# Kernel optimization log

Measured on AMD Instinct MI355X. Metric: run time of the kernel, lower is better.

## Reference

```python
import jax, jax.numpy as jnp
import numpy as np

DIM = 1024
HEADS = 16
HEAD_DIM = DIM // HEADS  # 64
EPS = 1e-5


def layer_norm(x, w, b):
    # LayerNorm over last dim (head_dim), matching nn.LayerNorm defaults
    mu = jnp.mean(x, axis=-1, keepdims=True)
    var = jnp.mean(jnp.square(x - mu), axis=-1, keepdims=True)
    return (x - mu) * jax.lax.rsqrt(var + EPS) * w + b


def apply_rotary_emb(x, freqs):
    # x: [B, S, H, D]; freqs: [S, D/2] angles. Interleaved (complex) rotary:
    # pairs (x[2i], x[2i+1]) rotated by angle freqs[:, i].
    x1 = x[..., 0::2]
    x2 = x[..., 1::2]
    cos = jnp.cos(freqs)[None, :, None, :]
    sin = jnp.sin(freqs)[None, :, None, :]
    r1 = x1 * cos - x2 * sin
    r2 = x1 * sin + x2 * cos
    return jnp.stack([r1, r2], axis=-1).reshape(x.shape)


def setup_inputs() -> dict:
    key = jax.random.key(0)
    ks = jax.random.split(key, 8)
    B, S = 2, 2048
    x = jax.random.normal(ks[0], (B, S, DIM), dtype=jnp.float32)
    freqs = jax.random.uniform(ks[1], (S, HEAD_DIM // 2), dtype=jnp.float32)
    sc = 1.0 / np.sqrt(DIM)
    w_qkv = jax.random.normal(ks[2], (DIM, 4 * DIM), dtype=jnp.float32) * sc
    w_out = jax.random.normal(ks[3], (DIM, DIM), dtype=jnp.float32) * sc
    qn_w = jnp.ones((HEAD_DIM,), jnp.float32)
    qn_b = jnp.zeros((HEAD_DIM,), jnp.float32)
    kn_w = jnp.ones((HEAD_DIM,), jnp.float32)
    kn_b = jnp.zeros((HEAD_DIM,), jnp.float32)
    return {"x": x, "freqs": freqs, "w_qkv": w_qkv, "w_out": w_out,
            "qn_w": qn_w, "qn_b": qn_b, "kn_w": kn_w, "kn_b": kn_b}


def reference(x, freqs, w_qkv, w_out, qn_w, qn_b, kn_w, kn_b):
    B, S, _ = x.shape
    qkv = x @ w_qkv  # [B, S, 4*DIM]
    q, k, v, gate = jnp.split(qkv, 4, axis=-1)
    q = q.reshape(B, S, HEADS, HEAD_DIM)
    k = k.reshape(B, S, HEADS, HEAD_DIM)
    v = v.reshape(B, S, HEADS, HEAD_DIM)
    q = layer_norm(q, qn_w, qn_b)
    k = layer_norm(k, kn_w, kn_b)
    q = apply_rotary_emb(q, freqs)
    k = apply_rotary_emb(k, freqs)
    # flash_attn_func: non-causal softmax attention, scale 1/sqrt(head_dim)
    scale = 1.0 / np.sqrt(HEAD_DIM)
    scores = jnp.einsum('bqhd,bkhd->bhqk', q, k) * scale
    probs = jax.nn.softmax(scores, axis=-1)
    o = jnp.einsum('bhqk,bkhd->bqhd', probs, v)
    o = o.reshape(B, S, DIM)
    o = o * jax.nn.sigmoid(gate)
    return o @ w_out
```

## Files before the change

kernel.cpp:

```cpp
#include <hip/hip_runtime.h>


typedef _Float16 f16;
typedef _Float16 f16x8 __attribute__((ext_vector_type(8)));
typedef _Float16 f16x4 __attribute__((ext_vector_type(4)));
typedef float    f32x4 __attribute__((ext_vector_type(4)));

#define MFMA16(a, b, c) __builtin_amdgcn_mfma_f32_16x16x32_f16((a), (b), (c), 0, 0, 0)

__device__ __forceinline__ void gload16(const void* g, void* l) {
  __builtin_amdgcn_global_load_lds(
      (const __attribute__((address_space(1))) void*)g,
      (__attribute__((address_space(3))) void*)l, 16, 0, 0);
}

__device__ __forceinline__ float exp2_fast(float x) {
#if __has_builtin(__builtin_amdgcn_exp2f)
  return __builtin_amdgcn_exp2f(x);
#else
  float r;
  asm("v_exp_f32 %0, %1" : "=v"(r) : "v"(x));
  return r;
#endif
}
__device__ __forceinline__ unsigned pkrtz(float a, float b) {
  typedef __fp16 hf16x2 __attribute__((ext_vector_type(2)));
  union { hf16x2 h; unsigned u; } c;
  c.h = __builtin_amdgcn_cvt_pkrtz(a, b);
  return c.u;
}

__global__ void rope_table_kernel(const float* __restrict__ freqs, float* __restrict__ tbl) {
  int i = blockIdx.x * 256 + threadIdx.x;
  if (i >= 2048 * 32) return;
  int s = i >> 5, j = i & 31;
  float f = freqs[i];
  tbl[s * 64 + j]      = cosf(f);
  tbl[s * 64 + 32 + j] = sinf(f);
}

__global__ void cast_f16_kernel(const float* __restrict__ in, f16* __restrict__ out, int n8) {
  int i = blockIdx.x * 256 + threadIdx.x;
  if (i >= n8) return;
  float4 a = ((const float4*)in)[2 * i];
  float4 b = ((const float4*)in)[2 * i + 1];
  f16x8 o;
  o[0] = (f16)a.x; o[1] = (f16)a.y; o[2] = (f16)a.z; o[3] = (f16)a.w;
  o[4] = (f16)b.x; o[5] = (f16)b.y; o[6] = (f16)b.z; o[7] = (f16)b.w;
  ((f16x8*)out)[i] = o;
}

__global__ void transpose_cast_kernel(const float* __restrict__ in, f16* __restrict__ out,
                                      int R, int C) {
  __shared__ float t[64][65];
  int c0 = blockIdx.x * 64, r0 = blockIdx.y * 64;
  int tx = threadIdx.x & 15, ty = threadIdx.x >> 4;
#pragma unroll
  for (int i = 0; i < 4; ++i) {
    float4 v = *(const float4*)&in[(size_t)(r0 + ty + 16 * i) * C + c0 + tx * 4];
    t[ty + 16 * i][tx * 4 + 0] = v.x;
    t[ty + 16 * i][tx * 4 + 1] = v.y;
    t[ty + 16 * i][tx * 4 + 2] = v.z;
    t[ty + 16 * i][tx * 4 + 3] = v.w;
  }
  __syncthreads();
#pragma unroll
  for (int i = 0; i < 4; ++i) {
    int n = c0 + ty + 16 * i;
    int k = r0 + tx * 4;
    f16x4 o;
    o[0] = (f16)t[tx * 4 + 0][ty + 16 * i];
    o[1] = (f16)t[tx * 4 + 1][ty + 16 * i];
    o[2] = (f16)t[tx * 4 + 2][ty + 16 * i];
    o[3] = (f16)t[tx * 4 + 3][ty + 16 * i];
    *(f16x4*)&out[(size_t)n * R + k] = o;
  }
}

__global__ void fill_debug_kernel(float* out, int n) {
  int i = blockIdx.x * 256 + threadIdx.x;
  if (i < n) out[i] = 12345.0f;
}

__global__ __launch_bounds__(512, 1) void gemm_qkv_256(
    const f16* __restrict__ A, const f16* __restrict__ B, int K,
    f16* __restrict__ qraw, f16* __restrict__ kraw,
    f16* __restrict__ g16, f16* __restrict__ v_t) {
  __shared__ f16 sA[2][256 * 64], sB[2][256 * 64];
  const int tid = threadIdx.x, lane = tid & 63;
  const int wave = tid >> 6;
  const int wm = wave >> 2, wn = wave & 3;
  const int lg = lane >> 4, lr = lane & 15;
  const int n0 = blockIdx.x * 256, m0 = blockIdx.y * 256;

  auto stg = [&](int k0, int p) {
#pragma unroll
    for (int r = 0; r < 4; ++r) {
      int off = (tid + r * 512) * 16;
      int row = off >> 7;
      int col = ((off & 127) ^ ((row & 7) << 4)) >> 1;
      gload16(A + (size_t)(m0 + row) * K + k0 + col, (char*)sA[p] + off);
      gload16(B + (size_t)(n0 + row) * K + k0 + col, (char*)sB[p] + off);
    }
  };

  f32x4 acc[8][4];
#pragma unroll
  for (int m = 0; m < 8; ++m)
#pragma unroll
    for (int n = 0; n < 4; ++n) acc[m][n] = (f32x4){0.f, 0.f, 0.f, 0.f};

  stg(0, 0);
  const int NT = K >> 6;
  int cur = 0;
  for (int t = 0; t < NT; ++t, cur ^= 1) {
    __syncthreads();
    if (t + 1 < NT) stg((t + 1) << 6, cur ^ 1);
#pragma unroll
    for (int ks = 0; ks < 2; ++ks) {
      f16x8 bfr[4];
#pragma unroll
      for (int n = 0; n < 4; ++n) {
        int row = wn * 64 + n * 16 + lr;
        int boff = (row << 7) + (ks << 6) + (lg << 4);
        boff ^= (row & 7) << 4;
        bfr[n] = *(const f16x8*)((const char*)sB[cur] + boff);
      }
#pragma unroll
      for (int m = 0; m < 8; ++m) {
        int row = wm * 128 + m * 16 + lr;
        int aoff = (row << 7) + (ks << 6) + (lg << 4);
        aoff ^= (row & 7) << 4;
        f16x8 afr = *(const f16x8*)((const char*)sA[cur] + aoff);
#pragma unroll
        for (int n = 0; n < 4; ++n) acc[m][n] = MFMA16(afr, bfr[n], acc[m][n]);
      }
    }
  }

  const int region = n0 >> 10;
  if (region == 2) {
#pragma unroll
    for (int m = 0; m < 8; ++m) {
      int row = m0 + wm * 128 + m * 16 + 4 * lg;
#pragma unroll
      for (int n = 0; n < 4; ++n) {
        int c = (n0 & 1023) + wn * 64 + n * 16 + lr;
        int hh = c >> 6, d = c & 63;
        int bb = row >> 11, s = row & 2047;
        f16x4 pv;
        pv[0] = (f16)acc[m][n][0];
        pv[1] = (f16)acc[m][n][1];
        pv[2] = (f16)acc[m][n][2];
        pv[3] = (f16)acc[m][n][3];
        *(f16x4*)&v_t[(size_t)((bb * 16 + hh) * 64 + d) * 2048 + s] = pv;
      }
    }
  } else if (region == 3) {
#pragma unroll
    for (int m = 0; m < 8; ++m) {
      int row = m0 + wm * 128 + m * 16 + 4 * lg;
#pragma unroll
      for (int n = 0; n < 4; ++n) {
        int col = (n0 & 1023) + wn * 64 + n * 16 + lr;
#pragma unroll
        for (int r = 0; r < 4; ++r) {
          float sg = 1.0f / (1.0f + exp2_fast(acc[m][n][r] * -1.44269504f));
          g16[(size_t)(row + r) * 1024 + col] = (f16)sg;
        }
      }
    }
  } else {
    f16* dst = region ? kraw : qraw;
#pragma unroll
    for (int m = 0; m < 8; ++m) {
      int row = m0 + wm * 128 + m * 16 + 4 * lg;
#pragma unroll
      for (int n = 0; n < 4; ++n) {
        int col = (n0 & 1023) + wn * 64 + n * 16 + lr;
#pragma unroll
        for (int r = 0; r < 4; ++r)
          dst[(size_t)(row + r) * 1024 + col] = (f16)acc[m][n][r];
      }
    }
  }
}

__global__ __launch_bounds__(256, 2) void gemm_out_128(
    const f16* __restrict__ A, const f16* __restrict__ B,
    float* __restrict__ Cout, int M, int N, int K) {
  __shared__ f16 sA[2][128 * 64], sB[2][128 * 64];
  const int tid = threadIdx.x, lane = tid & 63;
  const int wave = tid >> 6, wm = wave >> 1, wn = wave & 1;
  const int lg = lane >> 4, lr = lane & 15;
  const int n0 = blockIdx.x * 128, m0 = blockIdx.y * 128;

  auto stg = [&](int k0, int p) {
#pragma unroll
    for (int r = 0; r < 4; ++r) {
      int off = (tid + r * 256) * 16;
      int row = off >> 7;
      int col = ((off & 127) ^ ((row & 7) << 4)) >> 1;
      gload16(A + (size_t)(m0 + row) * K + k0 + col, (char*)sA[p] + off);
      gload16(B + (size_t)(n0 + row) * K + k0 + col, (char*)sB[p] + off);
    }
  };

  f32x4 acc[4][4];
#pragma unroll
  for (int m = 0; m < 4; ++m)
#pragma unroll
    for (int n = 0; n < 4; ++n) acc[m][n] = (f32x4){0.f, 0.f, 0.f, 0.f};

  stg(0, 0);
  const int NT = K >> 6;
  int cur = 0;
  for (int t = 0; t < NT; ++t, cur ^= 1) {
    __syncthreads();
    if (t + 1 < NT) stg((t + 1) << 6, cur ^ 1);
#pragma unroll
    for (int ks = 0; ks < 2; ++ks) {
      f16x8 bfr[4];
#pragma unroll
      for (int n = 0; n < 4; ++n) {
        int row = wn * 64 + n * 16 + lr;
        int boff = (row << 7) + (ks << 6) + (lg << 4);
        boff ^= (row & 7) << 4;
        bfr[n] = *(const f16x8*)((const char*)sB[cur] + boff);
      }
#pragma unroll
      for (int m = 0; m < 4; ++m) {
        int row = wm * 64 + m * 16 + lr;
        int aoff = (row << 7) + (ks << 6) + (lg << 4);
        aoff ^= (row & 7) << 4;
        f16x8 afr = *(const f16x8*)((const char*)sA[cur] + aoff);
#pragma unroll
        for (int n = 0; n < 4; ++n) acc[m][n] = MFMA16(afr, bfr[n], acc[m][n]);
      }
    }
  }

#pragma unroll
  for (int m = 0; m < 4; ++m) {
    int row = m0 + wm * 64 + m * 16 + 4 * lg;
#pragma unroll
    for (int n = 0; n < 4; ++n) {
      int col = n0 + wn * 64 + n * 16 + lr;
#pragma unroll
      for (int r = 0; r < 4; ++r) Cout[(size_t)(row + r) * N + col] = acc[m][n][r];
    }
  }
}

__global__ void norm_rope16_kernel(const f16* __restrict__ qr, const f16* __restrict__ kr,
                                   const float* __restrict__ tbl,
                                   const float* __restrict__ qn_w, const float* __restrict__ qn_b,
                                   const float* __restrict__ kn_w, const float* __restrict__ kn_b,
                                   f16* __restrict__ q_h, f16* __restrict__ k_h) {
  int row = blockIdx.x;
  int s = row & 2047;
  int hh = threadIdx.x >> 4, sub = threadIdx.x & 15;
  int base = row * 1024 + hh * 64 + sub * 4;
  float c0 = tbl[s * 64 + sub * 2 + 0], c1 = tbl[s * 64 + sub * 2 + 1];
  float s0 = tbl[s * 64 + 32 + sub * 2 + 0], s1 = tbl[s * 64 + 32 + sub * 2 + 1];
#pragma unroll
  for (int which = 0; which < 2; ++which) {
    const f16* src = which ? kr : qr;
    const float* wp = which ? kn_w : qn_w;
    const float* bp = which ? kn_b : qn_b;
    f16* dst = which ? k_h : q_h;
    f16x4 xr = *(const f16x4*)&src[base];
    float x0 = (float)xr[0], x1 = (float)xr[1], x2 = (float)xr[2], x3 = (float)xr[3];
    float sum = x0 + x1 + x2 + x3;
    sum += __shfl_xor(sum, 1); sum += __shfl_xor(sum, 2);
    sum += __shfl_xor(sum, 4); sum += __shfl_xor(sum, 8);
    float mu = sum * (1.0f / 64.0f);
    float d0 = x0 - mu, d1 = x1 - mu, d2 = x2 - mu, d3 = x3 - mu;
    float sq = d0 * d0 + d1 * d1 + d2 * d2 + d3 * d3;
    sq += __shfl_xor(sq, 1); sq += __shfl_xor(sq, 2);
    sq += __shfl_xor(sq, 4); sq += __shfl_xor(sq, 8);
    float rstd = rsqrtf(sq * (1.0f / 64.0f) + 1e-5f);
    float4 w = *(const float4*)&wp[sub * 4];
    float4 bb = *(const float4*)&bp[sub * 4];
    float n0 = d0 * rstd * w.x + bb.x;
    float n1 = d1 * rstd * w.y + bb.y;
    float n2 = d2 * rstd * w.z + bb.z;
    float n3 = d3 * rstd * w.w + bb.w;
    float r0 = n0 * c0 - n1 * s0, r1 = n0 * s0 + n1 * c0;
    float r2 = n2 * c1 - n3 * s1, r3 = n2 * s1 + n3 * c1;
    f16x4 ov;
    ov[0] = (f16)r0; ov[1] = (f16)r1; ov[2] = (f16)r2; ov[3] = (f16)r3;
    *(f16x4*)&dst[base] = ov;
  }
}

__global__ __launch_bounds__(256, 2) void attn_kernel(const f16* __restrict__ q_h,
                                                      const f16* __restrict__ k_h,
                                                      const f16* __restrict__ v_t,
                                                      const f16* __restrict__ g16,
                                                      f16* __restrict__ a16) {
  __shared__ __align__(16) char smem[65536];
  const int tid = threadIdx.x, lane = tid & 63, wave = tid >> 6;
  const int lg = lane >> 4, lr = lane & 15;
  const int bh = blockIdx.x >> 4, qt = blockIdx.x & 15;
  const int b = bh >> 4, h = bh & 15;
  const int qrow0 = b * 2048 + qt * 128 + wave * 32;

  auto stage = [&](int kv0, int p) {
    char* kb = smem + p * 16384;
    char* vb = smem + 32768 + p * 16384;
#pragma unroll
    for (int r = 0; r < 4; ++r) {
      int off = (tid + r * 256) * 16;
      {
        int row = off >> 7;
        int col = ((off & 127) ^ ((row & 7) << 4)) >> 1;
        int g = ((row >> 5) << 5) + (((row >> 2) & 3) << 3) + (((row >> 4) & 1) << 2) + (row & 3);
        gload16(&k_h[(size_t)(b * 2048 + kv0 + g) * 1024 + h * 64 + col], kb + off);
      }
      {
        int d = off >> 8;
        int col = ((off & 255) ^ ((d & 15) << 4)) >> 1;
        gload16(&v_t[(size_t)(bh * 64 + d) * 2048 + kv0 + col], vb + off);
      }
    }
  };

  f16x8 qf[2][2];
#pragma unroll
  for (int n = 0; n < 2; ++n)
#pragma unroll
    for (int ks = 0; ks < 2; ++ks)
      qf[n][ks] = *(const f16x8*)&q_h[(size_t)(qrow0 + n * 16 + lr) * 1024 + h * 64 + ks * 32 + lg * 8];

  f16x8 ones;
#pragma unroll
  for (int j = 0; j < 8; ++j) ones[j] = (f16)1.0f;

  f32x4 accO[4][2];
#pragma unroll
  for (int m = 0; m < 4; ++m) {
    accO[m][0] = (f32x4){0.f, 0.f, 0.f, 0.f};
    accO[m][1] = (f32x4){0.f, 0.f, 0.f, 0.f};
  }
  f32x4 accL[2] = {(f32x4){0.f, 0.f, 0.f, 0.f}, (f32x4){0.f, 0.f, 0.f, 0.f}};
  float mrun[2] = {-1e30f, -1e30f};
  const float SCL2 = 0.125f * 1.44269504f;
  const float THRP = 44.36f;
  const f32x4 fz = (f32x4){0.f, 0.f, 0.f, 0.f};

  stage(0, 0);

  int cur = 0;
  for (int t = 0; t < 16; ++t, cur ^= 1) {
    __syncthreads();
    if (t < 15) stage((t + 1) * 128, cur ^ 1);

    const char* kb = smem + cur * 16384;
    const char* vb = smem + 32768 + cur * 16384;

    f32x4 st[8][2];
    __builtin_amdgcn_s_setprio(1);
#pragma unroll
    for (int m = 0; m < 8; ++m) {
      int row = m * 16 + lr;
      int koff0 = ((row << 7) + (lg << 4)) ^ ((row & 7) << 4);
      int koff1 = ((row << 7) + 64 + (lg << 4)) ^ ((row & 7) << 4);
      f16x8 a0 = *(const f16x8*)(kb + koff0);
      f16x8 a1 = *(const f16x8*)(kb + koff1);
      st[m][0] = MFMA16(a1, qf[0][1], MFMA16(a0, qf[0][0], fz));
      st[m][1] = MFMA16(a1, qf[1][1], MFMA16(a0, qf[1][0], fz));
    }
    __builtin_amdgcn_s_setprio(0);

    uint2 pdw[2][8];
#pragma unroll
    for (int n = 0; n < 2; ++n) {
      float t03 = fmaxf(fmaxf(fmaxf(st[0][n][0], st[0][n][1]), fmaxf(st[0][n][2], st[0][n][3])),
                        fmaxf(fmaxf(st[1][n][0], st[1][n][1]), fmaxf(st[1][n][2], st[1][n][3])));
      float t47 = fmaxf(fmaxf(fmaxf(st[2][n][0], st[2][n][1]), fmaxf(st[2][n][2], st[2][n][3])),
                        fmaxf(fmaxf(st[3][n][0], st[3][n][1]), fmaxf(st[3][n][2], st[3][n][3])));
      float t8b = fmaxf(fmaxf(fmaxf(st[4][n][0], st[4][n][1]), fmaxf(st[4][n][2], st[4][n][3])),
                        fmaxf(fmaxf(st[5][n][0], st[5][n][1]), fmaxf(st[5][n][2], st[5][n][3])));
      float tcf = fmaxf(fmaxf(fmaxf(st[6][n][0], st[6][n][1]), fmaxf(st[6][n][2], st[6][n][3])),
                        fmaxf(fmaxf(st[7][n][0], st[7][n][1]), fmaxf(st[7][n][2], st[7][n][3])));
      float vm = fmaxf(fmaxf(t03, t47), fmaxf(t8b, tcf));
      vm = fmaxf(vm, __shfl_xor(vm, 16));
      vm = fmaxf(vm, __shfl_xor(vm, 32));
      if (__any(vm > mrun[n] + THRP)) {
        float mnew = fmaxf(mrun[n], vm);
        float fac = exp2_fast((mrun[n] - mnew) * SCL2);
        mrun[n] = mnew;
        accL[n] *= fac;
#pragma unroll
        for (int m = 0; m < 4; ++m) accO[m][n] *= fac;
      }
      float mc = mrun[n] * SCL2;
#pragma unroll
      for (int m = 0; m < 8; ++m) {
        float p0 = exp2_fast(st[m][n][0] * SCL2 - mc);
        float p1 = exp2_fast(st[m][n][1] * SCL2 - mc);
        float p2 = exp2_fast(st[m][n][2] * SCL2 - mc);
        float p3 = exp2_fast(st[m][n][3] * SCL2 - mc);
        pdw[n][m].x = pkrtz(p0, p1);
        pdw[n][m].y = pkrtz(p2, p3);
      }
    }

    f16x8 pb[2][4];
#pragma unroll
    for (int n = 0; n < 2; ++n)
#pragma unroll
      for (int ks = 0; ks < 4; ++ks) {
        union { uint4 u; f16x8 h; } c;
        c.u = make_uint4(pdw[n][2 * ks].x, pdw[n][2 * ks].y,
                         pdw[n][2 * ks + 1].x, pdw[n][2 * ks + 1].y);
        pb[n][ks] = c.h;
      }
    __builtin_amdgcn_s_setprio(1);
#pragma unroll
    for (int m = 0; m < 4; ++m)
#pragma unroll
      for (int ks = 0; ks < 4; ++ks) {
        int d = m * 16 + lr;
        int voff = (d << 8) + (ks << 6) + (lg << 4);
        voff ^= (d & 15) << 4;
        f16x8 av = *(const f16x8*)(vb + voff);
        accO[m][0] = MFMA16(av, pb[0][ks], accO[m][0]);
        accO[m][1] = MFMA16(av, pb[1][ks], accO[m][1]);
      }
#pragma unroll
    for (int ks = 0; ks < 4; ++ks) {
      accL[0] = MFMA16(ones, pb[0][ks], accL[0]);
      accL[1] = MFMA16(ones, pb[1][ks], accL[1]);
    }
    __builtin_amdgcn_s_setprio(0);
  }

#pragma unroll
  for (int n = 0; n < 2; ++n) {
    float rl = 1.0f / accL[n][0];
    int orow = qrow0 + n * 16 + lr;
#pragma unroll
    for (int m = 0; m < 4; ++m) {
      size_t idx = (size_t)orow * 1024 + h * 64 + m * 16 + lg * 4;
      f16x4 gv = *(const f16x4*)&g16[idx];
      f16x4 ov;
      ov[0] = (f16)(accO[m][n][0] * rl * (float)gv[0]);
      ov[1] = (f16)(accO[m][n][1] * rl * (float)gv[1]);
      ov[2] = (f16)(accO[m][n][2] * rl * (float)gv[2]);
      ov[3] = (f16)(accO[m][n][3] * rl * (float)gv[3]);
      *(f16x4*)&a16[idx] = ov;
    }
  }
}

extern "C" void kernel_launch(void* const* d_in, const int* in_sizes, int n_in,
                              void* d_out, int out_size, void* d_ws, size_t ws_size,
                              hipStream_t stream) {
  const float* x      = (const float*)d_in[0];
  const float* freqs  = (const float*)d_in[1];
  const float* w_qkv  = (const float*)d_in[2];
  const float* w_out  = (const float*)d_in[3];
  const float* qn_w   = (const float*)d_in[4];
  const float* qn_b   = (const float*)d_in[5];
  const float* kn_w   = (const float*)d_in[6];
  const float* kn_b   = (const float*)d_in[7];
  float* out = (float*)d_out;
  char* ws = (char*)d_ws;
  const size_t MB = 1024 * 1024;
  f16*   v_t   = (f16*)(ws + 0);
  f16*   x16   = (f16*)(ws + 8 * MB);
  f16*   wq16  = (f16*)(ws + 16 * MB);
  f16*   wo16  = (f16*)(ws + 24 * MB);
  f16*   qraw  = (f16*)(ws + 26 * MB);
  f16*   kraw  = (f16*)(ws + 34 * MB);
  f16*   q_h   = (f16*)(ws + 42 * MB);
  f16*   k_h   = (f16*)(ws + 50 * MB);
  f16*   g16   = (f16*)(ws + 58 * MB);
  float* tbl   = (float*)(ws + 66 * MB);
  f16*   a16   = x16;

  if (ws_size < (size_t)67 * MB) {
    fill_debug_kernel<<<(out_size + 255) / 256, 256, 0, stream>>>(out, out_size);
    return;
  }

  rope_table_kernel<<<256, 256, 0, stream>>>(freqs, tbl);
  cast_f16_kernel<<<2048, 256, 0, stream>>>(x, x16, 524288);
  transpose_cast_kernel<<<dim3(64, 16), 256, 0, stream>>>(w_qkv, wq16, 1024, 4096);
  transpose_cast_kernel<<<dim3(16, 16), 256, 0, stream>>>(w_out, wo16, 1024, 1024);

  gemm_qkv_256<<<dim3(16, 16), 512, 0, stream>>>(x16, wq16, 1024, qraw, kraw, g16, v_t);
  norm_rope16_kernel<<<4096, 256, 0, stream>>>(qraw, kraw, tbl, qn_w, qn_b, kn_w, kn_b, q_h, k_h);
  attn_kernel<<<512, 256, 0, stream>>>(q_h, k_h, v_t, g16, a16);
  gemm_out_128<<<dim3(8, 32), 256, 0, stream>>>(a16, wo16, out, 4096, 1024, 1024);
}
```

Measured before the change: 143.9 us.

## Use 4-stage K=32 LDS pipeline with vmcnt-gated barriers in QKV GEMM

The QKV projection GEMM moves from a double-buffered K=64 tile loop with a full __syncthreads per step to a 4-deep ring of K=32 stages, keeping three stages of global-to-LDS loads in flight. Each step waits only on the oldest stage's loads through s_waitcnt vmcnt before the barrier. The LDS layout is re-swizzled to pack two rows per 128-byte line, and the MFMA block is wrapped in s_setprio to favour compute waves. The loop is hard-coded for K=1024 (32 stages), so it breaks if K changes, and it doubles the number of barriers per K.

```diff
diff --git a/kernel.cpp b/kernel.cpp
--- a/kernel.cpp
+++ b/kernel.cpp
@@ -86,21 +86,36 @@
     const f16* __restrict__ A, const f16* __restrict__ B, int K,
     f16* __restrict__ qraw, f16* __restrict__ kraw,
     f16* __restrict__ g16, f16* __restrict__ v_t) {
-  __shared__ f16 sA[2][256 * 64], sB[2][256 * 64];
+  __shared__ f16 sA[4][8192], sB[4][8192];
   const int tid = threadIdx.x, lane = tid & 63;
   const int wave = tid >> 6;
   const int wm = wave >> 2, wn = wave & 3;
   const int lg = lane >> 4, lr = lane & 15;
   const int n0 = blockIdx.x * 256, m0 = blockIdx.y * 256;
-
-  auto stg = [&](int k0, int p) {
-#pragma unroll
-    for (int r = 0; r < 4; ++r) {
-      int off = (tid + r * 512) * 16;
-      int row = off >> 7;
-      int col = ((off & 127) ^ ((row & 7) << 4)) >> 1;
-      gload16(A + (size_t)(m0 + row) * K + k0 + col, (char*)sA[p] + off);
-      gload16(B + (size_t)(n0 + row) * K + k0 + col, (char*)sB[p] + off);
+  const f16* Abase = A + (size_t)m0 * K;
+  const f16* Bbase = B + (size_t)n0 * K;
+
+  int ldsoff[2];
+  size_t goff[2];
+#pragma unroll
+  for (int r = 0; r < 2; ++r) {
+    int off = (tid + r * 512) * 16;
+    int q = off >> 7;
+    int sl = ((off >> 4) & 7) ^ (q & 7);
+    int grow = q * 2 + (sl >> 2);
+    int kc = (sl & 3) * 8;
+    ldsoff[r] = off;
+    goff[r] = (size_t)grow * K + kc;
+  }
+
+  auto stage = [&](int u) {
+    char* pa = (char*)sA[u & 3];
+    char* pb = (char*)sB[u & 3];
+    const int kb = u * 32;
+#pragma unroll
+    for (int r = 0; r < 2; ++r) {
+      gload16(Abase + kb + goff[r], pa + ldsoff[r]);
+      gload16(Bbase + kb + goff[r], pb + ldsoff[r]);
     }
   };
 
@@ -110,33 +125,49 @@
 #pragma unroll
     for (int n = 0; n < 4; ++n) acc[m][n] = (f32x4){0.f, 0.f, 0.f, 0.f};
 
-  stg(0, 0);
-  const int NT = K >> 6;
-  int cur = 0;
-  for (int t = 0; t < NT; ++t, cur ^= 1) {
-    __syncthreads();
-    if (t + 1 < NT) stg((t + 1) << 6, cur ^ 1);
-#pragma unroll
-    for (int ks = 0; ks < 2; ++ks) {
-      f16x8 bfr[4];
-#pragma unroll
-      for (int n = 0; n < 4; ++n) {
-        int row = wn * 64 + n * 16 + lr;
-        int boff = (row << 7) + (ks << 6) + (lg << 4);
-        boff ^= (row & 7) << 4;
-        bfr[n] = *(const f16x8*)((const char*)sB[cur] + boff);
-      }
-#pragma unroll
-      for (int m = 0; m < 8; ++m) {
-        int row = wm * 128 + m * 16 + lr;
-        int aoff = (row << 7) + (ks << 6) + (lg << 4);
-        aoff ^= (row & 7) << 4;
-        f16x8 afr = *(const f16x8*)((const char*)sA[cur] + aoff);
-#pragma unroll
-        for (int n = 0; n < 4; ++n) acc[m][n] = MFMA16(afr, bfr[n], acc[m][n]);
-      }
-    }
-  }
+  auto compute = [&](int u) {
+    const char* pa = (const char*)sA[u & 3];
+    const char* pb = (const char*)sB[u & 3];
+    f16x8 bfr[4];
+#pragma unroll
+    for (int n = 0; n < 4; ++n) {
+      int row = wn * 64 + n * 16 + lr;
+      int q = row >> 1;
+      int s = (((row & 1) << 2) | lg) ^ (q & 7);
+      bfr[n] = *(const f16x8*)(pb + (q << 7) + (s << 4));
+    }
+    __builtin_amdgcn_s_setprio(1);
+#pragma unroll
+    for (int m = 0; m < 8; ++m) {
+      int row = wm * 128 + m * 16 + lr;
+      int q = row >> 1;
+      int s = (((row & 1) << 2) | lg) ^ (q & 7);
+      f16x8 afr = *(const f16x8*)(pa + (q << 7) + (s << 4));
+#pragma unroll
+      for (int n = 0; n < 4; ++n) acc[m][n] = MFMA16(afr, bfr[n], acc[m][n]);
+    }
+    __builtin_amdgcn_s_setprio(0);
+  };
+
+#define SYNCV(NSTR)                                          \
+  asm volatile("s_waitcnt vmcnt(" NSTR ")" ::: "memory");    \
+  __builtin_amdgcn_sched_barrier(0);                         \
+  __builtin_amdgcn_s_barrier();                              \
+  asm volatile("" ::: "memory");                             \
+  __builtin_amdgcn_sched_barrier(0);
+
+  stage(0);
+  stage(1);
+  stage(2);
+  for (int u = 0; u < 29; ++u) {
+    SYNCV("8")
+    stage(u + 3);
+    compute(u);
+  }
+  SYNCV("8")  compute(29);
+  SYNCV("4")  compute(30);
+  SYNCV("0")  compute(31);
+#undef SYNCV
 
   const int region = n0 >> 10;
   if (region == 2) {
```

Measured after the change: 151.0 us. 1.05x slower.

## Fuse Q layernorm+rope into attention prologue and shrink out-proj GEMM tile

Applied to the files above, without the earlier changes.

Q normalization and rotary embedding now run inside the attention kernel's prologue, computed from the raw Q in registers. This removes the separate write and re-read of the normalized Q buffer, and the K-side norm kernel now only processes K. The first K/V stage load is issued before the Q prologue so the two can overlap. Separately, the output projection GEMM tile drops from 128x128 to 128x64, doubling the grid to 512 blocks for better CU occupancy at the cost of more A-matrix reloads.

```diff
diff --git a/kernel.cpp b/kernel.cpp
--- a/kernel.cpp
+++ b/kernel.cpp
@@ -186,14 +186,14 @@
   }
 }
 
-__global__ __launch_bounds__(256, 2) void gemm_out_128(
+__global__ __launch_bounds__(256, 2) void gemm_out_128x64(
     const f16* __restrict__ A, const f16* __restrict__ B,
     float* __restrict__ Cout, int M, int N, int K) {
-  __shared__ f16 sA[2][128 * 64], sB[2][128 * 64];
+  __shared__ f16 sA[2][128 * 64], sB[2][64 * 64];
   const int tid = threadIdx.x, lane = tid & 63;
   const int wave = tid >> 6, wm = wave >> 1, wn = wave & 1;
   const int lg = lane >> 4, lr = lane & 15;
-  const int n0 = blockIdx.x * 128, m0 = blockIdx.y * 128;
+  const int n0 = blockIdx.x * 64, m0 = blockIdx.y * 128;
 
   auto stg = [&](int k0, int p) {
 #pragma unroll
@@ -202,15 +202,21 @@
       int row = off >> 7;
       int col = ((off & 127) ^ ((row & 7) << 4)) >> 1;
       gload16(A + (size_t)(m0 + row) * K + k0 + col, (char*)sA[p] + off);
+    }
+#pragma unroll
+    for (int r = 0; r < 2; ++r) {
+      int off = (tid + r * 256) * 16;
+      int row = off >> 7;
+      int col = ((off & 127) ^ ((row & 7) << 4)) >> 1;
       gload16(B + (size_t)(n0 + row) * K + k0 + col, (char*)sB[p] + off);
     }
   };
 
-  f32x4 acc[4][4];
+  f32x4 acc[4][2];
 #pragma unroll
   for (int m = 0; m < 4; ++m)
 #pragma unroll
-    for (int n = 0; n < 4; ++n) acc[m][n] = (f32x4){0.f, 0.f, 0.f, 0.f};
+    for (int n = 0; n < 2; ++n) acc[m][n] = (f32x4){0.f, 0.f, 0.f, 0.f};
 
   stg(0, 0);
   const int NT = K >> 6;
@@ -220,10 +226,10 @@
     if (t + 1 < NT) stg((t + 1) << 6, cur ^ 1);
 #pragma unroll
     for (int ks = 0; ks < 2; ++ks) {
-      f16x8 bfr[4];
-#pragma unroll
-      for (int n = 0; n < 4; ++n) {
-        int row = wn * 64 + n * 16 + lr;
+      f16x8 bfr[2];
+#pragma unroll
+      for (int n = 0; n < 2; ++n) {
+        int row = wn * 32 + n * 16 + lr;
         int boff = (row << 7) + (ks << 6) + (lg << 4);
         boff ^= (row & 7) << 4;
         bfr[n] = *(const f16x8*)((const char*)sB[cur] + boff);
@@ -235,7 +241,7 @@
         aoff ^= (row & 7) << 4;
         f16x8 afr = *(const f16x8*)((const char*)sA[cur] + aoff);
 #pragma unroll
-        for (int n = 0; n < 4; ++n) acc[m][n] = MFMA16(afr, bfr[n], acc[m][n]);
+        for (int n = 0; n < 2; ++n) acc[m][n] = MFMA16(afr, bfr[n], acc[m][n]);
       }
     }
   }
@@ -244,59 +250,53 @@
   for (int m = 0; m < 4; ++m) {
     int row = m0 + wm * 64 + m * 16 + 4 * lg;
 #pragma unroll
-    for (int n = 0; n < 4; ++n) {
-      int col = n0 + wn * 64 + n * 16 + lr;
+    for (int n = 0; n < 2; ++n) {
+      int col = n0 + wn * 32 + n * 16 + lr;
 #pragma unroll
       for (int r = 0; r < 4; ++r) Cout[(size_t)(row + r) * N + col] = acc[m][n][r];
     }
   }
 }
 
-__global__ void norm_rope16_kernel(const f16* __restrict__ qr, const f16* __restrict__ kr,
-                                   const float* __restrict__ tbl,
-                                   const float* __restrict__ qn_w, const float* __restrict__ qn_b,
-                                   const float* __restrict__ kn_w, const float* __restrict__ kn_b,
-                                   f16* __restrict__ q_h, f16* __restrict__ k_h) {
+__global__ void norm_k16_kernel(const f16* __restrict__ kr, const float* __restrict__ tbl,
+                                const float* __restrict__ kn_w, const float* __restrict__ kn_b,
+                                f16* __restrict__ k_h) {
   int row = blockIdx.x;
   int s = row & 2047;
   int hh = threadIdx.x >> 4, sub = threadIdx.x & 15;
   int base = row * 1024 + hh * 64 + sub * 4;
   float c0 = tbl[s * 64 + sub * 2 + 0], c1 = tbl[s * 64 + sub * 2 + 1];
   float s0 = tbl[s * 64 + 32 + sub * 2 + 0], s1 = tbl[s * 64 + 32 + sub * 2 + 1];
-#pragma unroll
-  for (int which = 0; which < 2; ++which) {
-    const f16* src = which ? kr : qr;
-    const float* wp = which ? kn_w : qn_w;
-    const float* bp = which ? kn_b : qn_b;
-    f16* dst = which ? k_h : q_h;
-    f16x4 xr = *(const f16x4*)&src[base];
-    float x0 = (float)xr[0], x1 = (float)xr[1], x2 = (float)xr[2], x3 = (float)xr[3];
-    float sum = x0 + x1 + x2 + x3;
-    sum += __shfl_xor(sum, 1); sum += __shfl_xor(sum, 2);
-    sum += __shfl_xor(sum, 4); sum += __shfl_xor(sum, 8);
-    float mu = sum * (1.0f / 64.0f);
-    float d0 = x0 - mu, d1 = x1 - mu, d2 = x2 - mu, d3 = x3 - mu;
-    float sq = d0 * d0 + d1 * d1 + d2 * d2 + d3 * d3;
-    sq += __shfl_xor(sq, 1); sq += __shfl_xor(sq, 2);
-    sq += __shfl_xor(sq, 4); sq += __shfl_xor(sq, 8);
-    float rstd = rsqrtf(sq * (1.0f / 64.0f) + 1e-5f);
-    float4 w = *(const float4*)&wp[sub * 4];
-    float4 bb = *(const float4*)&bp[sub * 4];
-    float n0 = d0 * rstd * w.x + bb.x;
-    float n1 = d1 * rstd * w.y + bb.y;
-    float n2 = d2 * rstd * w.z + bb.z;
-    float n3 = d3 * rstd * w.w + bb.w;
-    float r0 = n0 * c0 - n1 * s0, r1 = n0 * s0 + n1 * c0;
-    float r2 = n2 * c1 - n3 * s1, r3 = n2 * s1 + n3 * c1;
-    f16x4 ov;
-    ov[0] = (f16)r0; ov[1] = (f16)r1; ov[2] = (f16)r2; ov[3] = (f16)r3;
-    *(f16x4*)&dst[base] = ov;
-  }
-}
-
-__global__ __launch_bounds__(256, 2) void attn_kernel(const f16* __restrict__ q_h,
+  f16x4 xr = *(const f16x4*)&kr[base];
+  float x0 = (float)xr[0], x1 = (float)xr[1], x2 = (float)xr[2], x3 = (float)xr[3];
+  float sum = x0 + x1 + x2 + x3;
+  sum += __shfl_xor(sum, 1); sum += __shfl_xor(sum, 2);
+  sum += __shfl_xor(sum, 4); sum += __shfl_xor(sum, 8);
+  float mu = sum * (1.0f / 64.0f);
+  float d0 = x0 - mu, d1 = x1 - mu, d2 = x2 - mu, d3 = x3 - mu;
+  float sq = d0 * d0 + d1 * d1 + d2 * d2 + d3 * d3;
+  sq += __shfl_xor(sq, 1); sq += __shfl_xor(sq, 2);
+  sq += __shfl_xor(sq, 4); sq += __shfl_xor(sq, 8);
+  float rstd = rsqrtf(sq * (1.0f / 64.0f) + 1e-5f);
+  float4 w = *(const float4*)&kn_w[sub * 4];
+  float4 bb = *(const float4*)&kn_b[sub * 4];
+  float n0 = d0 * rstd * w.x + bb.x;
+  float n1 = d1 * rstd * w.y + bb.y;
+  float n2 = d2 * rstd * w.z + bb.z;
+  float n3 = d3 * rstd * w.w + bb.w;
+  float r0 = n0 * c0 - n1 * s0, r1 = n0 * s0 + n1 * c0;
+  float r2 = n2 * c1 - n3 * s1, r3 = n2 * s1 + n3 * c1;
+  f16x4 ov;
+  ov[0] = (f16)r0; ov[1] = (f16)r1; ov[2] = (f16)r2; ov[3] = (f16)r3;
+  *(f16x4*)&k_h[base] = ov;
+}
+
+__global__ __launch_bounds__(256, 2) void attn_kernel(const f16* __restrict__ qraw,
                                                       const f16* __restrict__ k_h,
                                                       const f16* __restrict__ v_t,
+                                                      const float* __restrict__ tbl,
+                                                      const float* __restrict__ qn_w,
+                                                      const float* __restrict__ qn_b,
                                                       const f16* __restrict__ g16,
                                                       f16* __restrict__ a16) {
   __shared__ __align__(16) char smem[65536];
@@ -326,12 +326,64 @@
     }
   };
 
+  stage(0, 0);
+
+  float wv[16], bv[16];
+#pragma unroll
+  for (int ks = 0; ks < 2; ++ks) {
+    float4 wa = *(const float4*)&qn_w[ks * 32 + lg * 8];
+    float4 wb = *(const float4*)&qn_w[ks * 32 + lg * 8 + 4];
+    float4 ba = *(const float4*)&qn_b[ks * 32 + lg * 8];
+    float4 bbv = *(const float4*)&qn_b[ks * 32 + lg * 8 + 4];
+    wv[ks * 8 + 0] = wa.x; wv[ks * 8 + 1] = wa.y; wv[ks * 8 + 2] = wa.z; wv[ks * 8 + 3] = wa.w;
+    wv[ks * 8 + 4] = wb.x; wv[ks * 8 + 5] = wb.y; wv[ks * 8 + 6] = wb.z; wv[ks * 8 + 7] = wb.w;
+    bv[ks * 8 + 0] = ba.x; bv[ks * 8 + 1] = ba.y; bv[ks * 8 + 2] = ba.z; bv[ks * 8 + 3] = ba.w;
+    bv[ks * 8 + 4] = bbv.x; bv[ks * 8 + 5] = bbv.y; bv[ks * 8 + 6] = bbv.z; bv[ks * 8 + 7] = bbv.w;
+  }
+
   f16x8 qf[2][2];
 #pragma unroll
-  for (int n = 0; n < 2; ++n)
+  for (int n = 0; n < 2; ++n) {
+    int row = qrow0 + n * 16 + lr;
+    f16x8 raw[2];
+    raw[0] = *(const f16x8*)&qraw[(size_t)row * 1024 + h * 64 + lg * 8];
+    raw[1] = *(const f16x8*)&qraw[(size_t)row * 1024 + h * 64 + 32 + lg * 8];
+    float x[16];
 #pragma unroll
     for (int ks = 0; ks < 2; ++ks)
-      qf[n][ks] = *(const f16x8*)&q_h[(size_t)(qrow0 + n * 16 + lr) * 1024 + h * 64 + ks * 32 + lg * 8];
+#pragma unroll
+      for (int j = 0; j < 8; ++j) x[ks * 8 + j] = (float)raw[ks][j];
+    float sum = 0.f;
+#pragma unroll
+    for (int i = 0; i < 16; ++i) sum += x[i];
+    sum += __shfl_xor(sum, 16);
+    sum += __shfl_xor(sum, 32);
+    float mu = sum * (1.0f / 64.0f);
+    float sq = 0.f;
+#pragma unroll
+    for (int i = 0; i < 16; ++i) { float d = x[i] - mu; sq += d * d; }
+    sq += __shfl_xor(sq, 16);
+    sq += __shfl_xor(sq, 32);
+    float rstd = rsqrtf(sq * (1.0f / 64.0f) + 1e-5f);
+    int srow = row & 2047;
+    const float* tb = tbl + srow * 64;
+#pragma unroll
+    for (int ks = 0; ks < 2; ++ks) {
+      float4 c4 = *(const float4*)&tb[ks * 16 + lg * 4];
+      float4 s4 = *(const float4*)&tb[32 + ks * 16 + lg * 4];
+      float cc[4] = {c4.x, c4.y, c4.z, c4.w};
+      float ss[4] = {s4.x, s4.y, s4.z, s4.w};
+      f16x8 o;
+#pragma unroll
+      for (int jj = 0; jj < 4; ++jj) {
+        float y0 = (x[ks * 8 + 2 * jj] - mu) * rstd * wv[ks * 8 + 2 * jj] + bv[ks * 8 + 2 * jj];
+        float y1 = (x[ks * 8 + 2 * jj + 1] - mu) * rstd * wv[ks * 8 + 2 * jj + 1] + bv[ks * 8 + 2 * jj + 1];
+        o[2 * jj]     = (f16)(y0 * cc[jj] - y1 * ss[jj]);
+        o[2 * jj + 1] = (f16)(y0 * ss[jj] + y1 * cc[jj]);
+      }
+      qf[n][ks] = o;
+    }
+  }
 
   f16x8 ones;
 #pragma unroll
@@ -348,8 +400,6 @@
   const float SCL2 = 0.125f * 1.44269504f;
   const float THRP = 44.36f;
   const f32x4 fz = (f32x4){0.f, 0.f, 0.f, 0.f};
-
-  stage(0, 0);
 
   int cur = 0;
   for (int t = 0; t < 16; ++t, cur ^= 1) {
@@ -475,7 +525,6 @@
   f16*   wo16  = (f16*)(ws + 24 * MB);
   f16*   qraw  = (f16*)(ws + 26 * MB);
   f16*   kraw  = (f16*)(ws + 34 * MB);
-  f16*   q_h   = (f16*)(ws + 42 * MB);
   f16*   k_h   = (f16*)(ws + 50 * MB);
   f16*   g16   = (f16*)(ws + 58 * MB);
   float* tbl   = (float*)(ws + 66 * MB);
@@ -492,7 +541,7 @@
   transpose_cast_kernel<<<dim3(16, 16), 256, 0, stream>>>(w_out, wo16, 1024, 1024);
 
   gemm_qkv_256<<<dim3(16, 16), 512, 0, stream>>>(x16, wq16, 1024, qraw, kraw, g16, v_t);
-  norm_rope16_kernel<<<4096, 256, 0, stream>>>(qraw, kraw, tbl, qn_w, qn_b, kn_w, kn_b, q_h, k_h);
-  attn_kernel<<<512, 256, 0, stream>>>(q_h, k_h, v_t, g16, a16);
-  gemm_out_128<<<dim3(8, 32), 256, 0, stream>>>(a16, wo16, out, 4096, 1024, 1024);
-}
+  norm_k16_kernel<<<4096, 256, 0, stream>>>(kraw, tbl, kn_w, kn_b, k_h);
+  attn_kernel<<<512, 256, 0, stream>>>(qraw, k_h, v_t, tbl, qn_w, qn_b, g16, a16);
+  gemm_out_128x64<<<dim3(16, 32), 256, 0, stream>>>(a16, wo16, out, 4096, 1024, 1024);
+}
```

New measurement: 141.7 us. About the same (-1.5%).
